# Performance work log

Hardware: AMD Instinct MI355X
Metric: run time of the kernel (lower is better)

Reference implementation:

```python
import jax, jax.numpy as jnp
import numpy as np

B, L, D, H = 2, 4096, 512, 8
HD = D // H
SCALE = 1.0 / (D / H) ** 0.5


def setup_inputs() -> dict:
    key = jax.random.key(0)
    ks = jax.random.split(key, 12)
    s = 0.02
    inp = {
        "q": jax.random.normal(ks[0], (B, L, D), jnp.float32),
        "k": jax.random.normal(ks[1], (B, L, D), jnp.float32),
        "v": jax.random.normal(ks[2], (B, L, D), jnp.float32),
        # causal mask, True = keep (masked_fill where mask == False)
        "mask": jnp.tril(jnp.ones((L, L), bool))[None, None, :, :],
        "Wq": jax.random.normal(ks[3], (D, D), jnp.float32) * s,
        "bq": jnp.zeros((D,), jnp.float32),
        "Wk": jax.random.normal(ks[4], (D, D), jnp.float32) * s,
        "bk": jnp.zeros((D,), jnp.float32),
        "Wv": jax.random.normal(ks[5], (D, D), jnp.float32) * s,
        "bv": jnp.zeros((D,), jnp.float32),
        "Wo": jax.random.normal(ks[6], (D, D), jnp.float32) * s,
        "bo": jnp.zeros((D,), jnp.float32),
    }
    return inp


def _split_heads(x):
    # [B, L, D] -> [B, H, L, HD]
    b, l, d = x.shape
    return x.reshape(b, l, H, HD).transpose(0, 2, 1, 3)


def reference(q, k, v, mask, Wq, bq, Wk, bk, Wv, bv, Wo, bo):
    # Dropout is inference-mode (identity), matching module.eval().
    qh = _split_heads(q @ Wq.T + bq)          # [B,H,L,HD]
    kh = _split_heads(k @ Wk.T + bk)          # [B,H,L,HD]
    vh = _split_heads(v @ Wv.T + bv)          # [B,H,L,HD]
    scores = jnp.einsum("bhqd,bhkd->bhqk", qh, kh) * SCALE
    scores = jnp.where(mask, scores, -jnp.inf)
    attn = jax.nn.softmax(scores, axis=-1)
    out = jnp.einsum("bhqk,bhkd->bhqd", attn, vh)  # [B,H,L,HD]
    out = out.transpose(0, 2, 1, 3).reshape(q.shape[0], q.shape[1], D)
    return out @ Wo.T + bo
```

## Files before the change

kernel.cpp:

```cpp
#include <hip/hip_runtime.h>

typedef __bf16 bf16;
typedef __bf16 bf16x4 __attribute__((ext_vector_type(4)));
typedef __bf16 bf16x8 __attribute__((ext_vector_type(8)));
typedef float  f32x4  __attribute__((ext_vector_type(4)));
typedef float  f32x16 __attribute__((ext_vector_type(16)));

#define NB   2
#define NL   4096
#define ND   512
#define NH   8
#define NHD  64

static __device__ __forceinline__ void g2l16(const bf16* g, bf16* l) {
    __builtin_amdgcn_global_load_lds(
        (const __attribute__((address_space(1))) unsigned int*)g,
        (__attribute__((address_space(3))) unsigned int*)l, 16, 0, 0);
}

__global__ __launch_bounds__(256) void cvt_all(
    const float* __restrict__ q, const float* __restrict__ k, const float* __restrict__ v,
    const float* __restrict__ Wq, const float* __restrict__ Wk,
    const float* __restrict__ Wv, const float* __restrict__ Wo,
    bf16* __restrict__ qb, bf16* __restrict__ kb, bf16* __restrict__ vb,
    bf16* __restrict__ wqb, bf16* __restrict__ wkb,
    bf16* __restrict__ wvb, bf16* __restrict__ wob)
{
    const int z = blockIdx.z;
    const float* src; bf16* dst; int n4;
    switch (z) {
        case 0: src = q;  dst = qb;  n4 = NB * NL * ND / 4; break;
        case 1: src = k;  dst = kb;  n4 = NB * NL * ND / 4; break;
        case 2: src = v;  dst = vb;  n4 = NB * NL * ND / 4; break;
        case 3: src = Wq; dst = wqb; n4 = ND * ND / 4; break;
        case 4: src = Wk; dst = wkb; n4 = ND * ND / 4; break;
        case 5: src = Wv; dst = wvb; n4 = ND * ND / 4; break;
        default: src = Wo; dst = wob; n4 = ND * ND / 4; break;
    }
    for (int i = blockIdx.x * 256 + threadIdx.x; i < n4; i += gridDim.x * 256) {
        const f32x4 a = *(const f32x4*)(src + (size_t)i * 4);
        bf16x4 o;
        #pragma unroll
        for (int j = 0; j < 4; ++j) o[j] = (bf16)a[j];
        *(bf16x4*)(dst + (size_t)i * 4) = o;
    }
}

__global__ __launch_bounds__(256) void proj_qkv(
    const bf16* __restrict__ qb, const bf16* __restrict__ kb, const bf16* __restrict__ vb,
    const bf16* __restrict__ wq, const bf16* __restrict__ wk, const bf16* __restrict__ wv,
    const float* __restrict__ biasq, const float* __restrict__ biask, const float* __restrict__ biasv,
    bf16* __restrict__ qh, bf16* __restrict__ kh, bf16* __restrict__ vt)
{
    const int z = blockIdx.z;
    const bf16* X     = (z == 0) ? qb : (z == 1) ? kb : vb;
    const bf16* W     = (z == 0) ? wq : (z == 1) ? wk : wv;
    const float* bias = (z == 0) ? biasq : (z == 1) ? biask : biasv;

    const int m0 = blockIdx.y * 128;
    const int n0 = blockIdx.x * 128;

    __shared__ bf16 As[2][128 * 32];
    __shared__ bf16 Bs[2][128 * 32];

    const int t    = threadIdx.x;
    const int lane = t & 63;
    const int wm   = (t >> 7) & 1;
    const int wn   = (t >> 6) & 1;
    const int quad = lane >> 4;
    const int l16  = lane & 15;

    auto stage = [&](int k0, int buf) {
        #pragma unroll
        for (int p = 0; p < 2; ++p) {
            const int id = p * 256 + t;
            const int r = id >> 2, s = id & 3;
            const int c = (s ^ (r & 3)) * 8;
            g2l16(X + (size_t)(m0 + r) * ND + k0 + c, As[buf] + id * 8);
            g2l16(W + (size_t)(n0 + r) * ND + k0 + c, Bs[buf] + id * 8);
        }
    };

    f32x4 acc[4][4] = {};
    stage(0, 0);

    for (int it = 0; it < 16; ++it) {
        __syncthreads();
        if (it + 1 < 16) stage((it + 1) * 32, (it + 1) & 1);

        const bf16* as = As[it & 1];
        const bf16* bs = Bs[it & 1];
        bf16x8 aF[4], bF[4];
        #pragma unroll
        for (int i = 0; i < 4; ++i) {
            const int ra = wm * 64 + i * 16 + l16;
            const int rb = wn * 64 + i * 16 + l16;
            aF[i] = *(const bf16x8*)(as + ra * 32 + (quad ^ (ra & 3)) * 8);
            bF[i] = *(const bf16x8*)(bs + rb * 32 + (quad ^ (rb & 3)) * 8);
        }
        #pragma unroll
        for (int mt = 0; mt < 4; ++mt)
            #pragma unroll
            for (int nt = 0; nt < 4; ++nt)
                acc[mt][nt] = __builtin_amdgcn_mfma_f32_16x16x32_bf16(
                    aF[mt], bF[nt], acc[mt][nt], 0, 0, 0);
    }

    const float oscale = (z == 0) ? 0.125f : 1.0f;
    #pragma unroll
    for (int nt = 0; nt < 4; ++nt) {
        const int col = n0 + wn * 64 + nt * 16 + l16;
        const float bb = bias[col];
        const int h = col >> 6, hd = col & 63;
        #pragma unroll
        for (int mt = 0; mt < 4; ++mt) {
            const int row0 = m0 + wm * 64 + mt * 16 + quad * 4;
            const int b = row0 >> 12;
            const int l = row0 & 4095;
            if (z == 2) {
                bf16x4 val;
                #pragma unroll
                for (int r = 0; r < 4; ++r) val[r] = (bf16)(acc[mt][nt][r] + bb);
                *(bf16x4*)(vt + ((size_t)(b * NH + h) * NHD + hd) * NL + l) = val;
            } else {
                bf16* dst = (z == 0) ? qh : kh;
                #pragma unroll
                for (int r = 0; r < 4; ++r)
                    dst[((size_t)(b * NH + h) * NL + (l + r)) * NHD + hd] =
                        (bf16)((acc[mt][nt][r] + bb) * oscale);
            }
        }
    }
}

#define PW 72
__global__ __launch_bounds__(256, 2) void attn(
    const bf16* __restrict__ qh, const bf16* __restrict__ kh,
    const bf16* __restrict__ vt, bf16* __restrict__ ao)
{
    const int bh  = blockIdx.y;
    const int b   = bh >> 3, h = bh & 7;
    const int qtA = blockIdx.x;
    const int qtB = 31 - blockIdx.x;
    const int nA  = 2 * qtA + 2;

    __shared__ bf16 smem[16384 + 4 * 32 * PW];

    const int t    = threadIdx.x;
    const int wave = t >> 6;
    const int lane = t & 63;
    const int l32  = lane & 31;
    const int half = lane >> 5;

    const bf16* Qg = qh + (size_t)bh * NL * NHD;
    const bf16* Kg = kh + (size_t)bh * NL * NHD;
    const bf16* Vg = vt + (size_t)bh * NHD * NL;

    #pragma unroll
    for (int p = 0; p < 8; ++p) {
        const int id = p * 256 + t;
        const int tile = id >> 10, r = (id >> 3) & 127, s = id & 7;
        const int q0 = (tile ? qtB : qtA) * 128;
        g2l16(Qg + (size_t)(q0 + r) * NHD + s * 8, smem + id * 8);
    }
    __syncthreads();

    bf16x8 qf[2][4];
    #pragma unroll
    for (int tile = 0; tile < 2; ++tile)
        #pragma unroll
        for (int c = 0; c < 4; ++c)
            qf[tile][c] = *(const bf16x8*)(smem + tile * 8192 +
                (wave * 32 + l32) * 64 + c * 16 + half * 8);
    __syncthreads();

    auto stage_kv = [&](int k0, int buf) {
        #pragma unroll
        for (int p = 0; p < 2; ++p) {
            const int id = p * 256 + t;
            const int r = id >> 3, s = id & 7;
            g2l16(Kg + (size_t)(k0 + r) * NHD + ((s ^ (r & 7)) * 8),
                  smem + buf * 4096 + id * 8);
            g2l16(Vg + (size_t)r * NL + k0 + ((s ^ (r & 7)) * 8),
                  smem + 8192 + buf * 4096 + id * 8);
        }
    };
    stage_kv(0, 0);

    f32x16 o_acc[2] = {};
    float l_lane = 0.f;

    for (int j = 0; j < 66; ++j) {
        const int phase = (j >= nA) ? 1 : 0;
        const int kvt   = phase ? (j - nA) : j;
        const int qt    = phase ? qtB : qtA;

        __syncthreads();

        if (j + 1 < 66) {
            const int jn  = j + 1;
            const int kvn = (jn >= nA) ? (jn - nA) : jn;
            stage_kv(kvn * 64, jn & 1);
        }

        if (j == nA) {
            const float lt = l_lane + __shfl_xor(l_lane, 32, 64);
            const float rcp = 1.0f / fmaxf(lt, 1e-20f);
            const int row = qtA * 128 + wave * 32 + l32;
            #pragma unroll
            for (int mt2 = 0; mt2 < 2; ++mt2)
                #pragma unroll
                for (int rr = 0; rr < 4; ++rr) {
                    const int hd = mt2 * 32 + rr * 8 + half * 4;
                    bf16x4 val;
                    #pragma unroll
                    for (int rb = 0; rb < 4; ++rb)
                        val[rb] = (bf16)(o_acc[mt2][rr * 4 + rb] * rcp);
                    *(bf16x4*)(ao + ((size_t)b * NL + row) * ND + h * NHD + hd) = val;
                }
            o_acc[0] = (f32x16)(0.f); o_acc[1] = (f32x16)(0.f);
            l_lane = 0.f;
        }

        const bf16* ks = smem + (j & 1) * 4096;
        const bf16* vs = smem + 8192 + (j & 1) * 4096;

        f32x16 sacc[2] = {};
        #pragma unroll
        for (int c = 0; c < 4; ++c) {
            #pragma unroll
            for (int mt = 0; mt < 2; ++mt) {
                const int row   = mt * 32 + l32;
                const int chunk = 2 * c + half;
                const bf16x8 kf = *(const bf16x8*)(ks + row * 64 + ((chunk ^ (row & 7)) * 8));
                sacc[mt] = __builtin_amdgcn_mfma_f32_32x32x16_bf16(
                    kf, qf[phase][c], sacc[mt], 0, 0, 0);
            }
        }

        const bool diag = (kvt >= 2 * qt);
        const int  dq   = kvt * 64 - qt * 128;
        const int  qrow_l = wave * 32 + l32;
        bf16* pw = smem + 16384 + wave * 32 * PW;
        #pragma unroll
        for (int mt = 0; mt < 2; ++mt) {
            #pragma unroll
            for (int rr = 0; rr < 4; ++rr) {
                const int kvb = mt * 32 + rr * 8 + half * 4;
                bf16x4 val;
                #pragma unroll
                for (int rb = 0; rb < 4; ++rb) {
                    float e;
                    if (diag && (dq + kvb + rb > qrow_l)) e = 0.f;
                    else e = __expf(sacc[mt][rr * 4 + rb]);
                    l_lane += e;
                    val[rb] = (bf16)e;
                }
                *(bf16x4*)(pw + l32 * PW + kvb) = val;
            }
        }

        #pragma unroll
        for (int c = 0; c < 4; ++c) {
            const bf16x8 pf = *(const bf16x8*)(pw + l32 * PW + c * 16 + half * 8);
            #pragma unroll
            for (int mt2 = 0; mt2 < 2; ++mt2) {
                const int row = mt2 * 32 + l32;
                const int u8  = 2 * c + half;
                const bf16x8 vf = *(const bf16x8*)(vs + row * 64 + ((u8 ^ (row & 7)) * 8));
                o_acc[mt2] = __builtin_amdgcn_mfma_f32_32x32x16_bf16(
                    vf, pf, o_acc[mt2], 0, 0, 0);
            }
        }
    }

    {
        const float lt = l_lane + __shfl_xor(l_lane, 32, 64);
        const float rcp = 1.0f / fmaxf(lt, 1e-20f);
        const int row = qtB * 128 + wave * 32 + l32;
        #pragma unroll
        for (int mt2 = 0; mt2 < 2; ++mt2)
            #pragma unroll
            for (int rr = 0; rr < 4; ++rr) {
                const int hd = mt2 * 32 + rr * 8 + half * 4;
                bf16x4 val;
                #pragma unroll
                for (int rb = 0; rb < 4; ++rb)
                    val[rb] = (bf16)(o_acc[mt2][rr * 4 + rb] * rcp);
                *(bf16x4*)(ao + ((size_t)b * NL + row) * ND + h * NHD + hd) = val;
            }
    }
}

__global__ __launch_bounds__(256) void out_proj(
    const bf16* __restrict__ ao, const bf16* __restrict__ wo,
    const float* __restrict__ bo, float* __restrict__ out)
{
    const int m0 = blockIdx.y * 128;
    const int n0 = blockIdx.x * 128;

    __shared__ bf16 As[2][128 * 32];
    __shared__ bf16 Bs[2][128 * 32];

    const int t    = threadIdx.x;
    const int lane = t & 63;
    const int wm   = (t >> 7) & 1;
    const int wn   = (t >> 6) & 1;
    const int quad = lane >> 4;
    const int l16  = lane & 15;

    auto stage = [&](int k0, int buf) {
        #pragma unroll
        for (int p = 0; p < 2; ++p) {
            const int id = p * 256 + t;
            const int r = id >> 2, s = id & 3;
            const int c = (s ^ (r & 3)) * 8;
            g2l16(ao + (size_t)(m0 + r) * ND + k0 + c, As[buf] + id * 8);
            g2l16(wo + (size_t)(n0 + r) * ND + k0 + c, Bs[buf] + id * 8);
        }
    };

    f32x4 acc[4][4] = {};
    stage(0, 0);

    for (int it = 0; it < 16; ++it) {
        __syncthreads();
        if (it + 1 < 16) stage((it + 1) * 32, (it + 1) & 1);

        const bf16* as = As[it & 1];
        const bf16* bs = Bs[it & 1];
        bf16x8 aF[4], bF[4];
        #pragma unroll
        for (int i = 0; i < 4; ++i) {
            const int ra = wm * 64 + i * 16 + l16;
            const int rb = wn * 64 + i * 16 + l16;
            aF[i] = *(const bf16x8*)(as + ra * 32 + (quad ^ (ra & 3)) * 8);
            bF[i] = *(const bf16x8*)(bs + rb * 32 + (quad ^ (rb & 3)) * 8);
        }
        #pragma unroll
        for (int mt = 0; mt < 4; ++mt)
            #pragma unroll
            for (int nt = 0; nt < 4; ++nt)
                acc[mt][nt] = __builtin_amdgcn_mfma_f32_16x16x32_bf16(
                    aF[mt], bF[nt], acc[mt][nt], 0, 0, 0);
    }

    #pragma unroll
    for (int nt = 0; nt < 4; ++nt) {
        const int col = n0 + wn * 64 + nt * 16 + l16;
        const float bb = bo[col];
        #pragma unroll
        for (int mt = 0; mt < 4; ++mt) {
            const int row0 = m0 + wm * 64 + mt * 16 + quad * 4;
            #pragma unroll
            for (int r = 0; r < 4; ++r)
                out[(size_t)(row0 + r) * ND + col] = acc[mt][nt][r] + bb;
        }
    }
}

extern "C" void kernel_launch(void* const* d_in, const int* in_sizes, int n_in,
                              void* d_out, int out_size, void* d_ws, size_t ws_size,
                              hipStream_t stream) {
    (void)in_sizes; (void)n_in; (void)out_size; (void)ws_size;

    const float* q  = (const float*)d_in[0];
    const float* k  = (const float*)d_in[1];
    const float* v  = (const float*)d_in[2];
    const float* Wq = (const float*)d_in[4];
    const float* bq = (const float*)d_in[5];
    const float* Wk = (const float*)d_in[6];
    const float* bk = (const float*)d_in[7];
    const float* Wv = (const float*)d_in[8];
    const float* bv = (const float*)d_in[9];
    const float* Wo = (const float*)d_in[10];
    const float* bo = (const float*)d_in[11];

    const size_t XSZ = (size_t)NB * NL * ND;
    const size_t WSZ = (size_t)ND * ND;
    bf16* p = (bf16*)d_ws;
    bf16* qb  = p; p += XSZ;
    bf16* kb  = p; p += XSZ;
    bf16* vb  = p; p += XSZ;
    bf16* wqb = p; p += WSZ;
    bf16* wkb = p; p += WSZ;
    bf16* wvb = p; p += WSZ;
    bf16* wob = p; p += WSZ;
    bf16* qh  = p; p += XSZ;
    bf16* kh  = p; p += XSZ;
    bf16* vt  = p; p += XSZ;
    bf16* ao  = p; p += XSZ;

    cvt_all<<<dim3(512, 1, 7), 256, 0, stream>>>(
        q, k, v, Wq, Wk, Wv, Wo, qb, kb, vb, wqb, wkb, wvb, wob);

    dim3 g1(ND / 128, (NB * NL) / 128, 3);
    proj_qkv<<<g1, 256, 0, stream>>>(qb, kb, vb, wqb, wkb, wvb, bq, bk, bv, qh, kh, vt);

    dim3 g2(16, NB * NH, 1);
    attn<<<g2, 256, 0, stream>>>(qh, kh, vt, ao);

    dim3 g3(ND / 128, (NB * NL) / 128, 1);
    out_proj<<<g3, 256, 0, stream>>>(ao, wob, bo, (float*)d_out);
}
```

Before: 268.9 us.

## Launch one attention block per query tile, heaviest first, and use exp2

Drops the paired-tile scheme, where each block handled q-tile i and 31-i to balance causal work. Now each block handles a single 128-row query tile, and blockIdx.y is reversed so the longest tiles are scheduled first. The grid doubles to 512 blocks, which improves occupancy and tail balance but reloads K/V for shorter work per block. It also folds log2(e) into the K projection scale so the softmax can use exp2f instead of __expf.

Result: slower. 282.4 us (+5.0%).

```diff
diff --git a/kernel.cpp b/kernel.cpp
--- a/kernel.cpp
+++ b/kernel.cpp
@@ -106,7 +106,7 @@
                     aF[mt], bF[nt], acc[mt][nt], 0, 0, 0);
     }
 
-    const float oscale = (z == 0) ? 0.125f : 1.0f;
+    const float oscale = (z == 0) ? 0.125f : (z == 1) ? 1.4426950408889634f : 1.0f;
     #pragma unroll
     for (int nt = 0; nt < 4; ++nt) {
         const int col = n0 + wn * 64 + nt * 16 + l16;
@@ -138,11 +138,11 @@
     const bf16* __restrict__ qh, const bf16* __restrict__ kh,
     const bf16* __restrict__ vt, bf16* __restrict__ ao)
 {
-    const int bh  = blockIdx.y;
-    const int b   = bh >> 3, h = bh & 7;
-    const int qtA = blockIdx.x;
-    const int qtB = 31 - blockIdx.x;
-    const int nA  = 2 * qtA + 2;
+    const int bh = blockIdx.x;
+    const int b  = bh >> 3, h = bh & 7;
+    const int qt = 31 - blockIdx.y;
+    const int q0 = qt * 128;
+    const int nkv = 2 * qt + 2;
 
     __shared__ bf16 smem[16384 + 4 * 32 * PW];
 
@@ -157,21 +157,17 @@
     const bf16* Vg = vt + (size_t)bh * NHD * NL;
 
     #pragma unroll
-    for (int p = 0; p < 8; ++p) {
+    for (int p = 0; p < 4; ++p) {
         const int id = p * 256 + t;
-        const int tile = id >> 10, r = (id >> 3) & 127, s = id & 7;
-        const int q0 = (tile ? qtB : qtA) * 128;
+        const int r = id >> 3, s = id & 7;
         g2l16(Qg + (size_t)(q0 + r) * NHD + s * 8, smem + id * 8);
     }
     __syncthreads();
 
-    bf16x8 qf[2][4];
+    bf16x8 qf[4];
     #pragma unroll
-    for (int tile = 0; tile < 2; ++tile)
-        #pragma unroll
-        for (int c = 0; c < 4; ++c)
-            qf[tile][c] = *(const bf16x8*)(smem + tile * 8192 +
-                (wave * 32 + l32) * 64 + c * 16 + half * 8);
+    for (int c = 0; c < 4; ++c)
+        qf[c] = *(const bf16x8*)(smem + (wave * 32 + l32) * 64 + c * 16 + half * 8);
     __syncthreads();
 
     auto stage_kv = [&](int k0, int buf) {
@@ -190,37 +186,9 @@
     f32x16 o_acc[2] = {};
     float l_lane = 0.f;
 
-    for (int j = 0; j < 66; ++j) {
-        const int phase = (j >= nA) ? 1 : 0;
-        const int kvt   = phase ? (j - nA) : j;
-        const int qt    = phase ? qtB : qtA;
-
+    for (int j = 0; j < nkv; ++j) {
         __syncthreads();
-
-        if (j + 1 < 66) {
-            const int jn  = j + 1;
-            const int kvn = (jn >= nA) ? (jn - nA) : jn;
-            stage_kv(kvn * 64, jn & 1);
-        }
-
-        if (j == nA) {
-            const float lt = l_lane + __shfl_xor(l_lane, 32, 64);
-            const float rcp = 1.0f / fmaxf(lt, 1e-20f);
-            const int row = qtA * 128 + wave * 32 + l32;
-            #pragma unroll
-            for (int mt2 = 0; mt2 < 2; ++mt2)
-                #pragma unroll
-                for (int rr = 0; rr < 4; ++rr) {
-                    const int hd = mt2 * 32 + rr * 8 + half * 4;
-                    bf16x4 val;
-                    #pragma unroll
-                    for (int rb = 0; rb < 4; ++rb)
-                        val[rb] = (bf16)(o_acc[mt2][rr * 4 + rb] * rcp);
-                    *(bf16x4*)(ao + ((size_t)b * NL + row) * ND + h * NHD + hd) = val;
-                }
-            o_acc[0] = (f32x16)(0.f); o_acc[1] = (f32x16)(0.f);
-            l_lane = 0.f;
-        }
+        if (j + 1 < nkv) stage_kv((j + 1) * 64, (j + 1) & 1);
 
         const bf16* ks = smem + (j & 1) * 4096;
         const bf16* vs = smem + 8192 + (j & 1) * 4096;
@@ -234,12 +202,12 @@
                 const int chunk = 2 * c + half;
                 const bf16x8 kf = *(const bf16x8*)(ks + row * 64 + ((chunk ^ (row & 7)) * 8));
                 sacc[mt] = __builtin_amdgcn_mfma_f32_32x32x16_bf16(
-                    kf, qf[phase][c], sacc[mt], 0, 0, 0);
-            }
-        }
-
-        const bool diag = (kvt >= 2 * qt);
-        const int  dq   = kvt * 64 - qt * 128;
+                    kf, qf[c], sacc[mt], 0, 0, 0);
+            }
+        }
+
+        const bool diag = (j >= 2 * qt);
+        const int  dq   = j * 64 - qt * 128;
         const int  qrow_l = wave * 32 + l32;
         bf16* pw = smem + 16384 + wave * 32 * PW;
         #pragma unroll
@@ -252,7 +220,7 @@
                 for (int rb = 0; rb < 4; ++rb) {
                     float e;
                     if (diag && (dq + kvb + rb > qrow_l)) e = 0.f;
-                    else e = __expf(sacc[mt][rr * 4 + rb]);
+                    else e = exp2f(sacc[mt][rr * 4 + rb]);
                     l_lane += e;
                     val[rb] = (bf16)e;
                 }
@@ -277,7 +245,7 @@
     {
         const float lt = l_lane + __shfl_xor(l_lane, 32, 64);
         const float rcp = 1.0f / fmaxf(lt, 1e-20f);
-        const int row = qtB * 128 + wave * 32 + l32;
+        const int row = q0 + wave * 32 + l32;
         #pragma unroll
         for (int mt2 = 0; mt2 < 2; ++mt2)
             #pragma unroll
@@ -397,7 +365,7 @@
     dim3 g1(ND / 128, (NB * NL) / 128, 3);
     proj_qkv<<<g1, 256, 0, stream>>>(qb, kb, vb, wqb, wkb, wvb, bq, bk, bv, qh, kh, vt);
 
-    dim3 g2(16, NB * NH, 1);
+    dim3 g2(16, 32, 1);
     attn<<<g2, 256, 0, stream>>>(qh, kh, vt, ao);
 
     dim3 g3(ND / 128, (NB * NL) / 128, 1);
```

## Split attention KV loop across two wave groups and fold log2e into K

Applied to the files above, without the earlier changes.

The attention block grows to 512 threads. Two 4-wave groups each handle half of the 66 KV tiles for the paired Q tiles, using separate double-buffered KV staging in LDS. Partial outputs and row sums from the second group are merged through LDS before the final normalise and store. K is also pre-scaled by log2(e) in the projection so exp2f replaces __expf. The intent is to halve the serial loop length per block and use more waves per CU, at the cost of doubled LDS use, a combine step, and possibly lower occupancy under the (512,2) launch bounds.

Result: faster. 259.2 us (-3.6%).

```diff
diff --git a/kernel.cpp b/kernel.cpp
--- a/kernel.cpp
+++ b/kernel.cpp
@@ -106,7 +106,7 @@
                     aF[mt], bF[nt], acc[mt][nt], 0, 0, 0);
     }
 
-    const float oscale = (z == 0) ? 0.125f : 1.0f;
+    const float oscale = (z == 0) ? 0.125f : (z == 1) ? 1.4426950408889634f : 1.0f;
     #pragma unroll
     for (int nt = 0; nt < 4; ++nt) {
         const int col = n0 + wn * 64 + nt * 16 + l16;
@@ -134,55 +134,59 @@
 }
 
 #define PW 72
-__global__ __launch_bounds__(256, 2) void attn(
+__global__ __launch_bounds__(512, 2) void attn(
     const bf16* __restrict__ qh, const bf16* __restrict__ kh,
     const bf16* __restrict__ vt, bf16* __restrict__ ao)
 {
-    const int bh  = blockIdx.y;
+    const int bh  = blockIdx.x;
     const int b   = bh >> 3, h = bh & 7;
-    const int qtA = blockIdx.x;
-    const int qtB = 31 - blockIdx.x;
+    const int qtA = blockIdx.y;
+    const int qtB = 31 - qtA;
     const int nA  = 2 * qtA + 2;
-
-    __shared__ bf16 smem[16384 + 4 * 32 * PW];
+    const int nB  = 2 * qtB + 2;
+
+    __shared__ bf16 smem[32768 + 8 * 32 * PW];
 
     const int t    = threadIdx.x;
     const int wave = t >> 6;
+    const int g    = wave >> 2;
+    const int w4   = wave & 3;
     const int lane = t & 63;
     const int l32  = lane & 31;
     const int half = lane >> 5;
+    const int sb   = g * 16384;
+    const int tg   = t & 255;
 
     const bf16* Qg = qh + (size_t)bh * NL * NHD;
     const bf16* Kg = kh + (size_t)bh * NL * NHD;
     const bf16* Vg = vt + (size_t)bh * NHD * NL;
 
     #pragma unroll
-    for (int p = 0; p < 8; ++p) {
-        const int id = p * 256 + t;
+    for (int p = 0; p < 4; ++p) {
+        const int id = p * 512 + t;
         const int tile = id >> 10, r = (id >> 3) & 127, s = id & 7;
         const int q0 = (tile ? qtB : qtA) * 128;
         g2l16(Qg + (size_t)(q0 + r) * NHD + s * 8, smem + id * 8);
     }
     __syncthreads();
 
-    bf16x8 qf[2][4];
+    bf16x8 qfA[4], qfB[4];
     #pragma unroll
-    for (int tile = 0; tile < 2; ++tile)
-        #pragma unroll
-        for (int c = 0; c < 4; ++c)
-            qf[tile][c] = *(const bf16x8*)(smem + tile * 8192 +
-                (wave * 32 + l32) * 64 + c * 16 + half * 8);
+    for (int c = 0; c < 4; ++c) {
+        qfA[c] = *(const bf16x8*)(smem +        (w4 * 32 + l32) * 64 + c * 16 + half * 8);
+        qfB[c] = *(const bf16x8*)(smem + 8192 + (w4 * 32 + l32) * 64 + c * 16 + half * 8);
+    }
     __syncthreads();
 
     auto stage_kv = [&](int k0, int buf) {
         #pragma unroll
         for (int p = 0; p < 2; ++p) {
-            const int id = p * 256 + t;
+            const int id = p * 256 + tg;
             const int r = id >> 3, s = id & 7;
             g2l16(Kg + (size_t)(k0 + r) * NHD + ((s ^ (r & 7)) * 8),
-                  smem + buf * 4096 + id * 8);
+                  smem + sb + buf * 8192 + id * 8);
             g2l16(Vg + (size_t)r * NL + k0 + ((s ^ (r & 7)) * 8),
-                  smem + 8192 + buf * 4096 + id * 8);
+                  smem + sb + buf * 8192 + 4096 + id * 8);
         }
     };
     stage_kv(0, 0);
@@ -190,23 +194,19 @@
     f32x16 o_acc[2] = {};
     float l_lane = 0.f;
 
-    for (int j = 0; j < 66; ++j) {
-        const int phase = (j >= nA) ? 1 : 0;
-        const int kvt   = phase ? (j - nA) : j;
-        const int qt    = phase ? qtB : qtA;
-
+    for (int jj = 0; jj < 33; ++jj) {
         __syncthreads();
 
-        if (j + 1 < 66) {
-            const int jn  = j + 1;
-            const int kvn = (jn >= nA) ? (jn - nA) : jn;
+        if (jj + 1 < 33) {
+            const int jn = jj + 1;
+            const int kvn = (g == 0) ? jn : (jn < nA ? jn : jn - nA + 33);
             stage_kv(kvn * 64, jn & 1);
         }
 
-        if (j == nA) {
+        if (g == 1 && jj == nA) {
             const float lt = l_lane + __shfl_xor(l_lane, 32, 64);
             const float rcp = 1.0f / fmaxf(lt, 1e-20f);
-            const int row = qtA * 128 + wave * 32 + l32;
+            const int row = qtA * 128 + w4 * 32 + l32;
             #pragma unroll
             for (int mt2 = 0; mt2 < 2; ++mt2)
                 #pragma unroll
@@ -222,26 +222,31 @@
             l_lane = 0.f;
         }
 
-        const bf16* ks = smem + (j & 1) * 4096;
-        const bf16* vs = smem + 8192 + (j & 1) * 4096;
+        const bool useA  = (g == 1) && (jj < nA);
+        const int j_glob = (g == 0) ? jj : (useA ? jj : jj - nA + 33);
+        const int qt_cur = useA ? qtA : qtB;
+
+        const bf16* ks = smem + sb + (jj & 1) * 8192;
+        const bf16* vs = ks + 4096;
 
         f32x16 sacc[2] = {};
         #pragma unroll
         for (int c = 0; c < 4; ++c) {
+            const bf16x8 qf = useA ? qfA[c] : qfB[c];
             #pragma unroll
             for (int mt = 0; mt < 2; ++mt) {
                 const int row   = mt * 32 + l32;
                 const int chunk = 2 * c + half;
                 const bf16x8 kf = *(const bf16x8*)(ks + row * 64 + ((chunk ^ (row & 7)) * 8));
                 sacc[mt] = __builtin_amdgcn_mfma_f32_32x32x16_bf16(
-                    kf, qf[phase][c], sacc[mt], 0, 0, 0);
+                    kf, qf, sacc[mt], 0, 0, 0);
             }
         }
 
-        const bool diag = (kvt >= 2 * qt);
-        const int  dq   = kvt * 64 - qt * 128;
-        const int  qrow_l = wave * 32 + l32;
-        bf16* pw = smem + 16384 + wave * 32 * PW;
+        const bool diag = (j_glob >= 2 * qt_cur);
+        const int  dq   = j_glob * 64 - qt_cur * 128;
+        const int  qrow_l = w4 * 32 + l32;
+        bf16* pw = smem + 32768 + wave * 32 * PW;
         #pragma unroll
         for (int mt = 0; mt < 2; ++mt) {
             #pragma unroll
@@ -252,7 +257,7 @@
                 for (int rb = 0; rb < 4; ++rb) {
                     float e;
                     if (diag && (dq + kvb + rb > qrow_l)) e = 0.f;
-                    else e = __expf(sacc[mt][rr * 4 + rb]);
+                    else e = exp2f(sacc[mt][rr * 4 + rb]);
                     l_lane += e;
                     val[rb] = (bf16)e;
                 }
@@ -274,10 +279,25 @@
         }
     }
 
-    {
+    __syncthreads();
+    float* comb = (float*)smem;
+    if (g == 1) {
+        const int base = w4 * (64 * 36) + lane * 36;
+        #pragma unroll
+        for (int mt2 = 0; mt2 < 2; ++mt2)
+            #pragma unroll
+            for (int i = 0; i < 16; ++i)
+                comb[base + mt2 * 16 + i] = o_acc[mt2][i];
         const float lt = l_lane + __shfl_xor(l_lane, 32, 64);
+        if (half == 0) comb[9216 + w4 * 32 + l32] = lt;
+    }
+    __syncthreads();
+    if (g == 0) {
+        const int base = w4 * (64 * 36) + lane * 36;
+        const float lt = l_lane + __shfl_xor(l_lane, 32, 64)
+                       + comb[9216 + w4 * 32 + l32];
         const float rcp = 1.0f / fmaxf(lt, 1e-20f);
-        const int row = qtB * 128 + wave * 32 + l32;
+        const int row = qtB * 128 + w4 * 32 + l32;
         #pragma unroll
         for (int mt2 = 0; mt2 < 2; ++mt2)
             #pragma unroll
@@ -286,7 +306,8 @@
                 bf16x4 val;
                 #pragma unroll
                 for (int rb = 0; rb < 4; ++rb)
-                    val[rb] = (bf16)(o_acc[mt2][rr * 4 + rb] * rcp);
+                    val[rb] = (bf16)((o_acc[mt2][rr * 4 + rb] +
+                                      comb[base + mt2 * 16 + rr * 4 + rb]) * rcp);
                 *(bf16x4*)(ao + ((size_t)b * NL + row) * ND + h * NHD + hd) = val;
             }
     }
@@ -397,8 +418,8 @@
     dim3 g1(ND / 128, (NB * NL) / 128, 3);
     proj_qkv<<<g1, 256, 0, stream>>>(qb, kb, vb, wqb, wkb, wvb, bq, bk, bv, qh, kh, vt);
 
-    dim3 g2(16, NB * NH, 1);
-    attn<<<g2, 256, 0, stream>>>(qh, kh, vt, ao);
+    dim3 g2(16, 16, 1);
+    attn<<<g2, 512, 0, stream>>>(qh, kh, vt, ao);
 
     dim3 g3(ND / 128, (NB * NL) / 128, 1);
     out_proj<<<g3, 256, 0, stream>>>(ao, wob, bo, (float*)d_out);
```
